# Kernel optimization log

Measured on AMD Instinct MI355X. Metric: run time of the kernel, lower is better.

Reference implementation:

```python
import jax, jax.numpy as jnp
import numpy as np


def setup_inputs() -> dict:
    key = jax.random.key(0)
    k1, k2 = jax.random.split(key)
    N, K, D = 32768, 1024, 512
    x = jax.random.normal(k1, (N, D), dtype=jnp.float32)
    centers = jax.random.normal(k2, (K, D), dtype=jnp.float32)
    return {"x": x, "centers": centers}


def reference(x, centers):
    # broadcasted (x[:,None]-c[None])**2 sum without the O(N*K*D) intermediate)
    x_sq = jnp.sum(x * x, axis=-1, keepdims=True)           # [N, 1]
    c_sq = jnp.sum(centers * centers, axis=-1)              # [K]
    cross = jnp.einsum('nd,kd->nk', x, centers)             # [N, K]
    norm_squared = x_sq + c_sq[None, :] - 2.0 * cross       # [N, K]
    # exp(-d/2) / sum_k exp(-d/2) == softmax(-d/2) over clusters
    probabilities = jax.nn.softmax(-0.5 * norm_squared, axis=1)
    return probabilities
```

## Files before the change

### kernel.cpp

```cpp
#include <hip/hip_runtime.h>
#include <stdint.h>


namespace {
constexpr int N_ROWS  = 32768;
constexpr int K_CL    = 1024;
constexpr int D_DIM   = 512;
constexpr int BM      = 64;
constexpr int THREADS = 512;
constexpr int WAVES   = 8;
constexpr int NSLICE  = 16;
}

typedef _Float16 f16_t;
typedef _Float16 f16x8 __attribute__((ext_vector_type(8)));
typedef _Float16 f16x4 __attribute__((ext_vector_type(4)));
typedef float    f32x16 __attribute__((ext_vector_type(16)));
typedef float    f32x4v __attribute__((ext_vector_type(4)));

__global__ __launch_bounds__(64) void prep_kernel(const float* __restrict__ centers,
                                                  f16_t* __restrict__ bpack,
                                                  float* __restrict__ bias) {
  const int col = blockIdx.x, lane = threadIdx.x;
  const int t  = lane >> 2;
  const int ks = (lane >> 1) & 1;
  const int kh = lane & 1;
  const float* src = centers + (size_t)col * D_DIM + lane * 8;
  f16x8 hi;
  float ssq = 0.f;
  #pragma unroll
  for (int i = 0; i < 8; ++i) {
    float v = src[i];
    ssq += v * v;
    hi[i] = (f16_t)v;
  }
  const int jh = col >> 9, cb = (col & 511) >> 5, c32 = col & 31;
  const size_t off = ((size_t)ks * 16 + cb) * 512 + (c32 * 2 + kh) * 8;
  *(f16x8*)(bpack + (size_t)(2 * t + jh) * 16384 + off) = hi;
  for (int o = 32; o; o >>= 1) ssq += __shfl_down(ssq, o, 64);
  if (lane == 0) bias[col] = -0.5f * ssq;
}

__global__ __launch_bounds__(THREADS, 2) void cluster_kernel(
    const float* __restrict__ x, const f16_t* __restrict__ bpack,
    const float* __restrict__ bias, float* __restrict__ out) {
  __shared__ __align__(16) char Ax[64 * 1024];
  __shared__ float red[WAVES * BM];
  __shared__ float fin[BM];

  const int tid  = threadIdx.x;
  const int wid  = tid >> 6;
  const int lane = tid & 63;
  const int l31  = lane & 31;
  const int h    = lane >> 5;
  const int brow = blockIdx.x * BM;

  const char* bbase = (const char*)bpack + wid * 2048 + (l31 * 2 + h) * 16;

#define LOADB8(S, DST)                                                         \
  {                                                                            \
    const char* p_ = bbase + (size_t)((S) & 31) * 32768;                       \
    (DST)[0] = *(const f16x8*)(p_);                       \
    (DST)[1] = *(const f16x8*)(p_ + 1024);                \
    (DST)[2] = *(const f16x8*)(p_ + 16384);               \
    (DST)[3] = *(const f16x8*)(p_ + 17408);               \
    (DST)[4] = *(const f16x8*)(p_ + 32768);               \
    (DST)[5] = *(const f16x8*)(p_ + 33792);               \
    (DST)[6] = *(const f16x8*)(p_ + 49152);               \
    (DST)[7] = *(const f16x8*)(p_ + 50176);               \
  }
#define COMPUTE16(B)                                                           \
  {                                                                            \
    _Pragma("unroll")                                                          \
    for (int j2_ = 0; j2_ < 2; ++j2_)                                          \
      _Pragma("unroll")                                                        \
      for (int ks_ = 0; ks_ < 2; ++ks_)                                        \
        _Pragma("unroll")                                                      \
        for (int c2_ = 0; c2_ < 2; ++c2_)                                      \
          _Pragma("unroll")                                                    \
          for (int rb_ = 0; rb_ < 2; ++rb_)                                    \
            acc[rb_][j2_ * 2 + c2_] = __builtin_amdgcn_mfma_f32_32x32x16_f16(  \
                a[rb_][ks_], (B)[j2_ * 4 + ks_ * 2 + c2_],                     \
                acc[rb_][j2_ * 2 + c2_], 0, 0, 0);                             \
  }

  f16x8 bA[8], bB[8];

  LOADB8(0, bA)

  {
    const float* xsrc = x + (size_t)brow * D_DIM;
    #pragma unroll
    for (int it = 0; it < 16; ++it) {
      const int idx = it * 512 + tid;
      const int r = idx >> 7, f = idx & 127;
      f32x4v v = __builtin_nontemporal_load(
          (const f32x4v*)(xsrc + (size_t)r * D_DIM + f * 4));
      f16x4 h4;
      h4[0] = (f16_t)v[0]; h4[1] = (f16_t)v[1];
      h4[2] = (f16_t)v[2]; h4[3] = (f16_t)v[3];
      *(f16x4*)(Ax + r * 1024 + ((f * 8) ^ ((r & 7) << 4))) = h4;
    }
  }
  __syncthreads();

  f32x16 acc[2][4];
  #pragma unroll
  for (int rb = 0; rb < 2; ++rb)
    #pragma unroll
    for (int cc = 0; cc < 4; ++cc)
      #pragma unroll
      for (int e = 0; e < 16; ++e) acc[rb][cc][e] = 0.f;

  const char* abase0 = Ax + l31 * 1024;
  const int swz = (l31 & 7) << 4;
  const int h16 = h * 16;
  f16x8 a[2][2];

  #pragma unroll
  for (int tt = 0; tt < 8; ++tt) {
    {
      const int T = 2 * tt;
      LOADB8(2 * (T + 1), bB)
      const int o0 = (T * 64 + h16) ^ swz;
      const int o1 = o0 ^ 32;
      a[0][0] = *(const f16x8*)(abase0 + o0);
      a[0][1] = *(const f16x8*)(abase0 + o1);
      a[1][0] = *(const f16x8*)(abase0 + 32768 + o0);
      a[1][1] = *(const f16x8*)(abase0 + 32768 + o1);
      COMPUTE16(bA)
    }
    {
      const int T = 2 * tt + 1;
      if (T < 15) LOADB8(2 * (T + 1), bA)
      const int o0 = (T * 64 + h16) ^ swz;
      const int o1 = o0 ^ 32;
      a[0][0] = *(const f16x8*)(abase0 + o0);
      a[0][1] = *(const f16x8*)(abase0 + o1);
      a[1][0] = *(const f16x8*)(abase0 + 32768 + o0);
      a[1][1] = *(const f16x8*)(abase0 + 32768 + o1);
      COMPUTE16(bB)
    }
  }

  float bcol[4];
  #pragma unroll
  for (int cc = 0; cc < 4; ++cc)
    bcol[cc] = bias[(cc >> 1) * 512 + wid * 64 + (cc & 1) * 32 + l31];

  float rr[2][16];
  #pragma unroll
  for (int rb = 0; rb < 2; ++rb)
    #pragma unroll
    for (int reg = 0; reg < 16; ++reg) {
      float m = -3.0e38f;
      #pragma unroll
      for (int cc = 0; cc < 4; ++cc) {
        float v = acc[rb][cc][reg] + bcol[cc];
        acc[rb][cc][reg] = v;
        m = fmaxf(m, v);
      }
      m = fmaxf(m, __shfl_xor(m, 1, 64));
      m = fmaxf(m, __shfl_xor(m, 2, 64));
      m = fmaxf(m, __shfl_xor(m, 4, 64));
      m = fmaxf(m, __shfl_xor(m, 8, 64));
      m = fmaxf(m, __shfl_xor(m, 16, 64));
      rr[rb][reg] = m;
    }
  __syncthreads();
  if (l31 == 0) {
    #pragma unroll
    for (int rb = 0; rb < 2; ++rb)
      #pragma unroll
      for (int reg = 0; reg < 16; ++reg)
        red[wid * BM + rb * 32 + (reg & 3) + 8 * (reg >> 2) + 4 * h] = rr[rb][reg];
  }
  __syncthreads();
  if (tid < BM) {
    float m = red[tid];
    #pragma unroll
    for (int w = 1; w < WAVES; ++w) m = fmaxf(m, red[w * BM + tid]);
    fin[tid] = m;
  }
  __syncthreads();

  #pragma unroll
  for (int rb = 0; rb < 2; ++rb)
    #pragma unroll
    for (int reg = 0; reg < 16; ++reg) {
      const float m = fin[rb * 32 + (reg & 3) + 8 * (reg >> 2) + 4 * h];
      float s = 0.f;
      #pragma unroll
      for (int cc = 0; cc < 4; ++cc) {
        float e = __expf(acc[rb][cc][reg] - m);
        acc[rb][cc][reg] = e;
        s += e;
      }
      s += __shfl_xor(s, 1, 64);
      s += __shfl_xor(s, 2, 64);
      s += __shfl_xor(s, 4, 64);
      s += __shfl_xor(s, 8, 64);
      s += __shfl_xor(s, 16, 64);
      rr[rb][reg] = s;
    }
  __syncthreads();
  if (l31 == 0) {
    #pragma unroll
    for (int rb = 0; rb < 2; ++rb)
      #pragma unroll
      for (int reg = 0; reg < 16; ++reg)
        red[wid * BM + rb * 32 + (reg & 3) + 8 * (reg >> 2) + 4 * h] = rr[rb][reg];
  }
  __syncthreads();
  if (tid < BM) {
    float s = 0.f;
    #pragma unroll
    for (int w = 0; w < WAVES; ++w) s += red[w * BM + tid];
    fin[tid] = 1.0f / s;
  }
  __syncthreads();

  #pragma unroll
  for (int rb = 0; rb < 2; ++rb)
    #pragma unroll
    for (int reg = 0; reg < 16; ++reg) {
      const int row = rb * 32 + (reg & 3) + 8 * (reg >> 2) + 4 * h;
      const float rs = fin[row];
      #pragma unroll
      for (int cc = 0; cc < 4; ++cc) {
        const int col = (cc >> 1) * 512 + wid * 64 + (cc & 1) * 32 + l31;
        __builtin_nontemporal_store(acc[rb][cc][reg] * rs,
                                    &out[(size_t)(brow + row) * K_CL + col]);
      }
    }
}

extern "C" void kernel_launch(void* const* d_in, const int* in_sizes, int n_in,
                              void* d_out, int out_size, void* d_ws, size_t ws_size,
                              hipStream_t stream) {
  const float* x       = (const float*)d_in[0];
  const float* centers = (const float*)d_in[1];
  float* out = (float*)d_out;

  f16_t* bpack = (f16_t*)d_ws;
  float* bias  = (float*)((char*)d_ws + (size_t)32 * 32768);

  prep_kernel<<<K_CL, 64, 0, stream>>>(centers, bpack, bias);
  cluster_kernel<<<N_ROWS / BM, THREADS, 0, stream>>>(x, bpack, bias, out);
}
```

Before: 89.23 us.

## Shrink row tile to 32 with 4 waves each covering 256 clusters

Halves the block row tile from 64 to 32 rows and the block from 8 to 4 waves. Each wave now computes one 32-row by 256-cluster strip with 8 accumulators instead of a 2x4 grid. This doubles the grid to 1024 blocks and halves shared memory per block, aiming at better occupancy and load balance. The cost is that each block reuses every B fragment for only 32 rows instead of 64, which doubles total B traffic from L2. The B prefetch is reordered to double-buffer across the two k-halves of each slice.

```diff
diff --git a/kernel.cpp b/kernel.cpp
--- a/kernel.cpp
+++ b/kernel.cpp
@@ -6,9 +6,8 @@
 constexpr int N_ROWS  = 32768;
 constexpr int K_CL    = 1024;
 constexpr int D_DIM   = 512;
-constexpr int BM      = 64;
-constexpr int THREADS = 512;
-constexpr int WAVES   = 8;
+constexpr int BM      = 32;
+constexpr int THREADS = 256;
 constexpr int NSLICE  = 16;
 }
 
@@ -44,55 +43,36 @@
 __global__ __launch_bounds__(THREADS, 2) void cluster_kernel(
     const float* __restrict__ x, const f16_t* __restrict__ bpack,
     const float* __restrict__ bias, float* __restrict__ out) {
-  __shared__ __align__(16) char Ax[64 * 1024];
-  __shared__ float red[WAVES * BM];
+  __shared__ __align__(16) char Ax[32768];
+  __shared__ float red[4 * BM];
   __shared__ float fin[BM];
 
   const int tid  = threadIdx.x;
-  const int wid  = tid >> 6;
+  const int w    = tid >> 6;
   const int lane = tid & 63;
   const int l31  = lane & 31;
   const int h    = lane >> 5;
   const int brow = blockIdx.x * BM;
 
-  const char* bbase = (const char*)bpack + wid * 2048 + (l31 * 2 + h) * 16;
-
-#define LOADB8(S, DST)                                                         \
+  const char* bbase = (const char*)bpack + (w >> 1) * 32768 + (w & 1) * 8192 +
+                      (l31 * 2 + h) * 16;
+
+#define LOADB(T, KS, DST)                                                      \
   {                                                                            \
-    const char* p_ = bbase + (size_t)((S) & 31) * 32768;                       \
-    (DST)[0] = *(const f16x8*)(p_);                       \
-    (DST)[1] = *(const f16x8*)(p_ + 1024);                \
-    (DST)[2] = *(const f16x8*)(p_ + 16384);               \
-    (DST)[3] = *(const f16x8*)(p_ + 17408);               \
-    (DST)[4] = *(const f16x8*)(p_ + 32768);               \
-    (DST)[5] = *(const f16x8*)(p_ + 33792);               \
-    (DST)[6] = *(const f16x8*)(p_ + 49152);               \
-    (DST)[7] = *(const f16x8*)(p_ + 50176);               \
-  }
-#define COMPUTE16(B)                                                           \
-  {                                                                            \
+    const char* p_ = bbase + (size_t)(T) * 65536 + (KS) * 16384;               \
     _Pragma("unroll")                                                          \
-    for (int j2_ = 0; j2_ < 2; ++j2_)                                          \
-      _Pragma("unroll")                                                        \
-      for (int ks_ = 0; ks_ < 2; ++ks_)                                        \
-        _Pragma("unroll")                                                      \
-        for (int c2_ = 0; c2_ < 2; ++c2_)                                      \
-          _Pragma("unroll")                                                    \
-          for (int rb_ = 0; rb_ < 2; ++rb_)                                    \
-            acc[rb_][j2_ * 2 + c2_] = __builtin_amdgcn_mfma_f32_32x32x16_f16(  \
-                a[rb_][ks_], (B)[j2_ * 4 + ks_ * 2 + c2_],                     \
-                acc[rb_][j2_ * 2 + c2_], 0, 0, 0);                             \
-  }
-
-  f16x8 bA[8], bB[8];
-
-  LOADB8(0, bA)
+    for (int cb_ = 0; cb_ < 8; ++cb_)                                          \
+      (DST)[cb_] = *(const f16x8*)(p_ + cb_ * 1024);                           \
+  }
+
+  f16x8 b0[8], b1[8];
+  LOADB(0, 0, b0)
 
   {
     const float* xsrc = x + (size_t)brow * D_DIM;
     #pragma unroll
     for (int it = 0; it < 16; ++it) {
-      const int idx = it * 512 + tid;
+      const int idx = it * 256 + tid;
       const int r = idx >> 7, f = idx & 127;
       f32x4v v = __builtin_nontemporal_load(
           (const f32x4v*)(xsrc + (size_t)r * D_DIM + f * 4));
@@ -104,135 +84,110 @@
   }
   __syncthreads();
 
-  f32x16 acc[2][4];
-  #pragma unroll
-  for (int rb = 0; rb < 2; ++rb)
-    #pragma unroll
-    for (int cc = 0; cc < 4; ++cc)
-      #pragma unroll
-      for (int e = 0; e < 16; ++e) acc[rb][cc][e] = 0.f;
-
-  const char* abase0 = Ax + l31 * 1024;
+  f32x16 acc[8];
+  #pragma unroll
+  for (int cb = 0; cb < 8; ++cb)
+    #pragma unroll
+    for (int e = 0; e < 16; ++e) acc[cb][e] = 0.f;
+
+  const char* abase = Ax + l31 * 1024;
   const int swz = (l31 & 7) << 4;
-  const int h16 = h * 16;
-  f16x8 a[2][2];
-
-  #pragma unroll
-  for (int tt = 0; tt < 8; ++tt) {
-    {
-      const int T = 2 * tt;
-      LOADB8(2 * (T + 1), bB)
-      const int o0 = (T * 64 + h16) ^ swz;
-      const int o1 = o0 ^ 32;
-      a[0][0] = *(const f16x8*)(abase0 + o0);
-      a[0][1] = *(const f16x8*)(abase0 + o1);
-      a[1][0] = *(const f16x8*)(abase0 + 32768 + o0);
-      a[1][1] = *(const f16x8*)(abase0 + 32768 + o1);
-      COMPUTE16(bA)
-    }
-    {
-      const int T = 2 * tt + 1;
-      if (T < 15) LOADB8(2 * (T + 1), bA)
-      const int o0 = (T * 64 + h16) ^ swz;
-      const int o1 = o0 ^ 32;
-      a[0][0] = *(const f16x8*)(abase0 + o0);
-      a[0][1] = *(const f16x8*)(abase0 + o1);
-      a[1][0] = *(const f16x8*)(abase0 + 32768 + o0);
-      a[1][1] = *(const f16x8*)(abase0 + 32768 + o1);
-      COMPUTE16(bB)
-    }
-  }
-
-  float bcol[4];
-  #pragma unroll
-  for (int cc = 0; cc < 4; ++cc)
-    bcol[cc] = bias[(cc >> 1) * 512 + wid * 64 + (cc & 1) * 32 + l31];
-
-  float rr[2][16];
-  #pragma unroll
-  for (int rb = 0; rb < 2; ++rb)
-    #pragma unroll
-    for (int reg = 0; reg < 16; ++reg) {
-      float m = -3.0e38f;
-      #pragma unroll
-      for (int cc = 0; cc < 4; ++cc) {
-        float v = acc[rb][cc][reg] + bcol[cc];
-        acc[rb][cc][reg] = v;
-        m = fmaxf(m, v);
-      }
-      m = fmaxf(m, __shfl_xor(m, 1, 64));
-      m = fmaxf(m, __shfl_xor(m, 2, 64));
-      m = fmaxf(m, __shfl_xor(m, 4, 64));
-      m = fmaxf(m, __shfl_xor(m, 8, 64));
-      m = fmaxf(m, __shfl_xor(m, 16, 64));
-      rr[rb][reg] = m;
-    }
-  __syncthreads();
+
+  #pragma unroll
+  for (int T = 0; T < NSLICE; ++T) {
+    const f16x8 a0 = *(const f16x8*)(abase + ((T * 64 + h * 16) ^ swz));
+    const f16x8 a1 = *(const f16x8*)(abase + ((T * 64 + 32 + h * 16) ^ swz));
+    LOADB(T, 1, b1)
+    #pragma unroll
+    for (int cb = 0; cb < 8; ++cb)
+      acc[cb] = __builtin_amdgcn_mfma_f32_32x32x16_f16(a0, b0[cb], acc[cb],
+                                                       0, 0, 0);
+    if (T < 15) { LOADB(T + 1, 0, b0) }
+    #pragma unroll
+    for (int cb = 0; cb < 8; ++cb)
+      acc[cb] = __builtin_amdgcn_mfma_f32_32x32x16_f16(a1, b1[cb], acc[cb],
+                                                       0, 0, 0);
+  }
+
+  float bcol[8];
+  #pragma unroll
+  for (int cb = 0; cb < 8; ++cb)
+    bcol[cb] = bias[w * 256 + cb * 32 + l31];
+
+  float rr[16];
+  #pragma unroll
+  for (int reg = 0; reg < 16; ++reg) {
+    float m = -3.0e38f;
+    #pragma unroll
+    for (int cb = 0; cb < 8; ++cb) {
+      float v = acc[cb][reg] + bcol[cb];
+      acc[cb][reg] = v;
+      m = fmaxf(m, v);
+    }
+    m = fmaxf(m, __shfl_xor(m, 1, 64));
+    m = fmaxf(m, __shfl_xor(m, 2, 64));
+    m = fmaxf(m, __shfl_xor(m, 4, 64));
+    m = fmaxf(m, __shfl_xor(m, 8, 64));
+    m = fmaxf(m, __shfl_xor(m, 16, 64));
+    rr[reg] = m;
+  }
   if (l31 == 0) {
     #pragma unroll
-    for (int rb = 0; rb < 2; ++rb)
-      #pragma unroll
-      for (int reg = 0; reg < 16; ++reg)
-        red[wid * BM + rb * 32 + (reg & 3) + 8 * (reg >> 2) + 4 * h] = rr[rb][reg];
+    for (int reg = 0; reg < 16; ++reg)
+      red[w * BM + (reg & 3) + 8 * (reg >> 2) + 4 * h] = rr[reg];
   }
   __syncthreads();
   if (tid < BM) {
     float m = red[tid];
     #pragma unroll
-    for (int w = 1; w < WAVES; ++w) m = fmaxf(m, red[w * BM + tid]);
+    for (int ww = 1; ww < 4; ++ww) m = fmaxf(m, red[ww * BM + tid]);
     fin[tid] = m;
   }
   __syncthreads();
 
   #pragma unroll
-  for (int rb = 0; rb < 2; ++rb)
-    #pragma unroll
-    for (int reg = 0; reg < 16; ++reg) {
-      const float m = fin[rb * 32 + (reg & 3) + 8 * (reg >> 2) + 4 * h];
-      float s = 0.f;
-      #pragma unroll
-      for (int cc = 0; cc < 4; ++cc) {
-        float e = __expf(acc[rb][cc][reg] - m);
-        acc[rb][cc][reg] = e;
-        s += e;
-      }
-      s += __shfl_xor(s, 1, 64);
-      s += __shfl_xor(s, 2, 64);
-      s += __shfl_xor(s, 4, 64);
-      s += __shfl_xor(s, 8, 64);
-      s += __shfl_xor(s, 16, 64);
-      rr[rb][reg] = s;
-    }
+  for (int reg = 0; reg < 16; ++reg) {
+    const float m = fin[(reg & 3) + 8 * (reg >> 2) + 4 * h];
+    float s = 0.f;
+    #pragma unroll
+    for (int cb = 0; cb < 8; ++cb) {
+      float e = __expf(acc[cb][reg] - m);
+      acc[cb][reg] = e;
+      s += e;
+    }
+    s += __shfl_xor(s, 1, 64);
+    s += __shfl_xor(s, 2, 64);
+    s += __shfl_xor(s, 4, 64);
+    s += __shfl_xor(s, 8, 64);
+    s += __shfl_xor(s, 16, 64);
+    rr[reg] = s;
+  }
   __syncthreads();
   if (l31 == 0) {
     #pragma unroll
-    for (int rb = 0; rb < 2; ++rb)
-      #pragma unroll
-      for (int reg = 0; reg < 16; ++reg)
-        red[wid * BM + rb * 32 + (reg & 3) + 8 * (reg >> 2) + 4 * h] = rr[rb][reg];
+    for (int reg = 0; reg < 16; ++reg)
+      red[w * BM + (reg & 3) + 8 * (reg >> 2) + 4 * h] = rr[reg];
   }
   __syncthreads();
   if (tid < BM) {
     float s = 0.f;
     #pragma unroll
-    for (int w = 0; w < WAVES; ++w) s += red[w * BM + tid];
+    for (int ww = 0; ww < 4; ++ww) s += red[ww * BM + tid];
     fin[tid] = 1.0f / s;
   }
   __syncthreads();
 
   #pragma unroll
-  for (int rb = 0; rb < 2; ++rb)
-    #pragma unroll
-    for (int reg = 0; reg < 16; ++reg) {
-      const int row = rb * 32 + (reg & 3) + 8 * (reg >> 2) + 4 * h;
-      const float rs = fin[row];
-      #pragma unroll
-      for (int cc = 0; cc < 4; ++cc) {
-        const int col = (cc >> 1) * 512 + wid * 64 + (cc & 1) * 32 + l31;
-        __builtin_nontemporal_store(acc[rb][cc][reg] * rs,
-                                    &out[(size_t)(brow + row) * K_CL + col]);
-      }
-    }
+  for (int reg = 0; reg < 16; ++reg) {
+    const int row = (reg & 3) + 8 * (reg >> 2) + 4 * h;
+    const float rs = fin[row];
+    #pragma unroll
+    for (int cb = 0; cb < 8; ++cb) {
+      const int col = w * 256 + cb * 32 + l31;
+      __builtin_nontemporal_store(acc[cb][reg] * rs,
+                                  &out[(size_t)(brow + row) * K_CL + col]);
+    }
+  }
 }
 
 extern "C" void kernel_launch(void* const* d_in, const int* in_sizes, int n_in,
```

New measurement: 92.59 us. 3.8% more time.
